# Optimization experiments

Hardware: AMD Instinct MI355X
Metric: run time of the kernel (lower is better)

Reference implementation:

```python
import jax, jax.numpy as jnp
import numpy as np
from jax.scipy.linalg import solve_triangular

N, D, E = 100000, 128, 1600000
LAMDA, ALPHA = 0.5, 0.1


def setup_inputs() -> dict:
    key = jax.random.key(0)
    k1, k2, k3, k4, k5, k6 = jax.random.split(key, 6)
    x = jax.random.normal(k1, (N, D), dtype=jnp.float32)
    h0 = jax.random.normal(k2, (N, D), dtype=jnp.float32)
    # glorot_init range for the weight
    init_range = np.sqrt(6.0 / (D + D)).astype(np.float32)
    weight = jax.random.uniform(k3, (D, D), dtype=jnp.float32, minval=-init_range, maxval=init_range)
    adj_vals = jax.random.uniform(k4, (E,), dtype=jnp.float32)  # normalized adjacency values (positive)
    adj_rows = jax.random.randint(k5, (E,), 0, N, dtype=jnp.int32)
    adj_cols = jax.random.randint(k6, (E,), 0, N, dtype=jnp.int32)
    return {"x": x, "h0": h0, "weight": weight, "adj_vals": adj_vals,
            "adj_rows": adj_rows, "adj_cols": adj_cols, "l": 4}


def _ortho_norm(weight):
    d = weight.shape[1]
    wtw = weight.T @ weight + 1e-4 * jnp.eye(d, dtype=weight.dtype)
    L = jnp.linalg.cholesky(wtw)
    # weight @ inv(L).T == (solve(L, weight.T)).T
    return solve_triangular(L, weight.T, lower=True).T


def reference(x, h0, weight, adj_vals, adj_rows, adj_cols, l):
    theta = float(np.log(LAMDA / l + 1.0))
    w_ortho = _ortho_norm(weight)
    # sparse adjacency SpMM: hi[r] = sum_e adj_vals[e] * x[adj_cols[e]] for adj_rows[e]==r
    hi = jax.ops.segment_sum(adj_vals[:, None] * x[adj_cols], adj_rows, num_segments=x.shape[0])
    support = (1.0 - ALPHA) * hi + ALPHA * h0  # variant=False -> r == support
    out = theta * (support @ w_ortho) + (1.0 - theta) * support
    return jnp.tanh(out)  # residual=False
```

## Files before the change

### kernel.cpp

```cpp
#include <hip/hip_runtime.h>
#include <math.h>

#define D 128
#define NB 16
#define RPB 64
#define NBUK_MAX 1024
#define RPBUK 128
#define EPB 16384
#define ALPHA 0.1f
#define LAMDA 0.5f

__global__ __launch_bounds__(256) void wtw_kernel(const float* __restrict__ W,
                                                  float* __restrict__ A) {
    int idx = blockIdx.x * blockDim.x + threadIdx.x;
    if (idx >= D * D) return;
    int i = idx >> 7, j = idx & (D - 1);
    float acc = (i == j) ? 1e-4f : 0.0f;
#pragma unroll 4
    for (int k = 0; k < D; ++k) acc = fmaf(W[k * D + i], W[k * D + j], acc);
    A[idx] = acc;
}

__global__ __launch_bounds__(256) void prep_kernel(
        const int* __restrict__ rows, int* __restrict__ bcnt, int E, int nbuk, int nCnt,
        const float* __restrict__ x, unsigned short* __restrict__ xb, int nd, int nCvt,
        const float* __restrict__ W, float* __restrict__ A) {
    __shared__ int lcnt[NBUK_MAX];
    const int tid = threadIdx.x;
    const int blk = blockIdx.x;

    if (blk < nCnt) {
        const int e0 = blk * EPB;
        const int e1 = min(e0 + EPB, E);
        for (int i = tid; i < nbuk; i += 256) lcnt[i] = 0;
        __syncthreads();
        for (int e = e0 + tid * 4; e < e1; e += 1024) {
            if (e + 3 < e1) {
                int4 r = *reinterpret_cast<const int4*>(rows + e);
                atomicAdd(&lcnt[r.x >> 7], 1);
                atomicAdd(&lcnt[r.y >> 7], 1);
                atomicAdd(&lcnt[r.z >> 7], 1);
                atomicAdd(&lcnt[r.w >> 7], 1);
            } else {
                int lim = min(e + 4, e1);
                for (int k = e; k < lim; ++k) atomicAdd(&lcnt[rows[k] >> 7], 1);
            }
        }
        __syncthreads();
        for (int i = tid; i < nbuk; i += 256) {
            int c = lcnt[i];
            if (c) atomicAdd(&bcnt[i], c);
        }
    } else if (blk < nCnt + nCvt) {
        const int base = ((blk - nCnt) * 256 + tid) * 8;
        if (base + 7 < nd) {
            float4 a = *reinterpret_cast<const float4*>(x + base);
            float4 b = *reinterpret_cast<const float4*>(x + base + 4);
            unsigned r[8];
            const float* f = &a.x;
#pragma unroll
            for (int i = 0; i < 4; ++i) {
                unsigned u = __float_as_uint(f[i]);
                r[i] = (u + 0x7FFFu + ((u >> 16) & 1u)) >> 16;
            }
            const float* g = &b.x;
#pragma unroll
            for (int i = 0; i < 4; ++i) {
                unsigned u = __float_as_uint(g[i]);
                r[4 + i] = (u + 0x7FFFu + ((u >> 16) & 1u)) >> 16;
            }
            uint4 o;
            o.x = r[0] | (r[1] << 16);
            o.y = r[2] | (r[3] << 16);
            o.z = r[4] | (r[5] << 16);
            o.w = r[6] | (r[7] << 16);
            *reinterpret_cast<uint4*>(xb + base) = o;
        } else {
            for (int i = 0; i < 8 && base + i < nd; ++i) {
                unsigned u = __float_as_uint(x[base + i]);
                xb[base + i] = (unsigned short)((u + 0x7FFFu + ((u >> 16) & 1u)) >> 16);
            }
        }
    } else {
        int idx = (blk - nCnt - nCvt) * 256 + tid;
        if (idx < D * D) {
            int i = idx >> 7, j = idx & (D - 1);
            float acc = (i == j) ? 1e-4f : 0.0f;
#pragma unroll 4
            for (int k = 0; k < D; ++k) acc = fmaf(W[k * D + i], W[k * D + j], acc);
            A[idx] = acc;
        }
    }
}

__global__ __launch_bounds__(1024) void scan_bucket_kernel(const int* __restrict__ bcnt,
                                                           int* __restrict__ bbase,
                                                           int* __restrict__ gcur,
                                                           int nbuk) {
    __shared__ int ps[1024];
    const int tid = threadIdx.x;
    int v = (tid < nbuk) ? bcnt[tid] : 0;
    ps[tid] = v;
    __syncthreads();
    for (int off = 1; off < 1024; off <<= 1) {
        int t = (tid >= off) ? ps[tid - off] : 0;
        __syncthreads();
        ps[tid] += t;
        __syncthreads();
    }
    if (tid < nbuk) {
        int excl = ps[tid] - v;
        bbase[tid] = excl;
        gcur[tid]  = excl;
    }
}

__global__ __launch_bounds__(256) void pc_kernel(
        const int* __restrict__ rows, const int* __restrict__ cols,
        const float* __restrict__ vals, int* __restrict__ gcur,
        uint2* __restrict__ buk, int E, int nbuk, int nPart,
        const float* __restrict__ A_in, float* __restrict__ Lg) {
    __shared__ float smem[D * D];
    __shared__ float dinvS[NB];
    const int tid = threadIdx.x;

    if ((int)blockIdx.x < nPart) {
        int* lcnt  = (int*)smem;
        int* lbase = lcnt + NBUK_MAX;
        int* loff  = lbase + NBUK_MAX;
        const int e0 = blockIdx.x * EPB;
        const int e1 = min(e0 + EPB, E);
        for (int i = tid; i < nbuk; i += 256) { lcnt[i] = 0; loff[i] = 0; }
        __syncthreads();
        for (int e = e0 + tid * 4; e < e1; e += 1024) {
            if (e + 3 < e1) {
                int4 r = *reinterpret_cast<const int4*>(rows + e);
                atomicAdd(&lcnt[r.x >> 7], 1);
                atomicAdd(&lcnt[r.y >> 7], 1);
                atomicAdd(&lcnt[r.z >> 7], 1);
                atomicAdd(&lcnt[r.w >> 7], 1);
            } else {
                int lim = min(e + 4, e1);
                for (int k = e; k < lim; ++k) atomicAdd(&lcnt[rows[k] >> 7], 1);
            }
        }
        __syncthreads();
        for (int i = tid; i < nbuk; i += 256) {
            int c = lcnt[i];
            if (c) lbase[i] = atomicAdd(&gcur[i], c);
        }
        __syncthreads();
        for (int e = e0 + tid * 4; e < e1; e += 1024) {
            if (e + 3 < e1) {
                int4 r = *reinterpret_cast<const int4*>(rows + e);
                int4 c = *reinterpret_cast<const int4*>(cols + e);
                float4 v = *reinterpret_cast<const float4*>(vals + e);
                {
                    int b = r.x >> 7; int li = atomicAdd(&loff[b], 1);
                    buk[lbase[b] + li] = make_uint2((unsigned)c.x | ((unsigned)(r.x & 127) << 20), __float_as_uint(v.x));
                }
                {
                    int b = r.y >> 7; int li = atomicAdd(&loff[b], 1);
                    buk[lbase[b] + li] = make_uint2((unsigned)c.y | ((unsigned)(r.y & 127) << 20), __float_as_uint(v.y));
                }
                {
                    int b = r.z >> 7; int li = atomicAdd(&loff[b], 1);
                    buk[lbase[b] + li] = make_uint2((unsigned)c.z | ((unsigned)(r.z & 127) << 20), __float_as_uint(v.z));
                }
                {
                    int b = r.w >> 7; int li = atomicAdd(&loff[b], 1);
                    buk[lbase[b] + li] = make_uint2((unsigned)c.w | ((unsigned)(r.w & 127) << 20), __float_as_uint(v.w));
                }
            } else {
                int lim = min(e + 4, e1);
                for (int k = e; k < lim; ++k) {
                    int rr = rows[k];
                    int b = rr >> 7; int li = atomicAdd(&loff[b], 1);
                    buk[lbase[b] + li] = make_uint2((unsigned)cols[k] | ((unsigned)(rr & 127) << 20), __float_as_uint(vals[k]));
                }
            }
        }
    } else {
        float (*S)[D] = (float (*)[D])smem;
        const int tx = tid & 15;
        const int ty = tid >> 4;

        for (int i = tid; i < D * D; i += 256) smem[i] = A_in[i];
        __syncthreads();

        for (int s = 0; s < D / NB; ++s) {
            const int b = s * NB;
            for (int k = 0; k < NB; ++k) {
                float dk  = S[b + k][b + k];
                float a_i = S[b + k][b + tx];
                float a_j = S[b + k][b + ty];
                float lkk  = sqrtf(dk);
                float inv  = 1.0f / lkk;
                float invd = inv * inv;
                __syncthreads();
                if (ty == 0) {
                    if (tx == k)       { S[b + k][b + k] = lkk; dinvS[k] = inv; }
                    else if (tx > k)     S[b + k][b + tx] = a_i * inv;
                }
                if (ty > k && tx >= ty)
                    S[b + ty][b + tx] -= a_i * (a_j * invd);
                __syncthreads();
            }

            const int m = D - b - NB;
            if (m > 0 && tid < m) {
                const int r = b + NB + tid;
                float y[NB];
#pragma unroll
                for (int k = 0; k < NB; ++k) y[k] = S[b + k][r];
#pragma unroll
                for (int k = 0; k < NB; ++k) {
                    float acc = y[k];
#pragma unroll
                    for (int q = 0; q < NB; ++q)
                        if (q < k) acc -= S[b + q][b + k] * y[q];
                    y[k] = acc * dinvS[k];
                }
#pragma unroll
                for (int k = 0; k < NB; ++k) S[b + k][r] = y[k];
            }
            __syncthreads();

            const int nt = m >> 4;
            for (int tc = 0; tc < nt; ++tc) {
                for (int tr = tc; tr < nt; ++tr) {
                    const int c = b + NB + tc * 16 + ty;
                    const int r = b + NB + tr * 16 + tx;
                    if (r >= c) {
                        float acc = S[c][r];
#pragma unroll
                        for (int k = 0; k < NB; ++k)
                            acc -= S[b + k][r] * S[b + k][c];
                        S[c][r] = acc;
                    }
                }
            }
            __syncthreads();
        }

        for (int i = tid; i < D * D; i += 256) Lg[i] = smem[i];
    }
}

__global__ __launch_bounds__(256) void cs_kernel(
        const uint2* __restrict__ buk, const int* __restrict__ bbase,
        const int* __restrict__ bend, uint2* __restrict__ csr,
        int* __restrict__ rp, int n, int nBuk,
        const float* __restrict__ Lg, const float* __restrict__ W,
        const int* __restrict__ lp, float* __restrict__ Mg) {
    __shared__ float Lr[D][D + 1];
    const int tid = threadIdx.x;
    const int b = blockIdx.x;

    if (b < nBuk) {
        int* lcnt = (int*)&Lr[0][0];
        int* lofs = lcnt + RPBUK;
        const int start = bbase[b], end = bend[b];

        if (tid < RPBUK) lcnt[tid] = 0;
        __syncthreads();
        for (int j = start + tid; j < end; j += 256)
            atomicAdd(&lcnt[buk[j].x >> 20], 1);
        __syncthreads();
        if (tid < RPBUK) lofs[tid] = lcnt[tid];
        __syncthreads();
        for (int off = 1; off < RPBUK; off <<= 1) {
            int v = (tid < RPBUK && tid >= off) ? lofs[tid - off] : 0;
            __syncthreads();
            if (tid < RPBUK) lofs[tid] += v;
            __syncthreads();
        }
        if (tid < RPBUK) {
            int r = b * RPBUK + tid;
            if (r < n) rp[r] = start + lofs[tid];
            lofs[tid] -= lcnt[tid];
        }
        __syncthreads();
        for (int j = start + tid; j < end; j += 256) {
            uint2 e = buk[j];
            int rl = e.x >> 20;
            int pos = atomicAdd(&lofs[rl], 1);
            csr[start + pos] = make_uint2(e.x & 0xFFFFFu, e.y);
        }
    } else {
        const int c = b - nBuk;
        for (int idx = tid; idx < D * D; idx += 256) {
            int i = idx & (D - 1), j = idx >> 7;
            Lr[i][j] = Lg[j * D + i];
        }
        __syncthreads();

        const int lane = tid & 63;
        const float w_lo = W[c * D + lane];
        const float w_hi = W[c * D + 64 + lane];
        const float dinv_lo = 1.0f / Lr[lane][lane];
        const float dinv_hi = 1.0f / Lr[lane + 64][lane + 64];
        float y_lo = 0.0f, y_hi = 0.0f;

        for (int i = 0; i < D; ++i) {
            float l0 = Lr[i][lane];
            float l1 = Lr[i][lane + 64];
            float p = 0.0f;
            p += (lane < i)      ? l0 * y_lo : 0.0f;
            p += (lane + 64 < i) ? l1 * y_hi : 0.0f;
#pragma unroll
            for (int off = 32; off >= 1; off >>= 1) p += __shfl_xor(p, off);
            if (i < 64) {
                if (lane == i)      y_lo = (w_lo - p) * dinv_lo;
            } else {
                if (lane == i - 64) y_hi = (w_hi - p) * dinv_hi;
            }
        }

        if (tid < 64) {
            const float th = logf(LAMDA / (float)(*lp) + 1.0f);
            float m_lo = th * y_lo + ((c == lane)      ? (1.0f - th) : 0.0f);
            float m_hi = th * y_hi + ((c == lane + 64) ? (1.0f - th) : 0.0f);
            Mg[c * D + lane]      = m_lo;
            Mg[c * D + 64 + lane] = m_hi;
        }
    }
}

__global__ __launch_bounds__(256, 4) void fused_spmm_gemm_kernel(
        const unsigned short* __restrict__ xb,
        const float* __restrict__ h0,
        const uint2* __restrict__ csr,
        const int* __restrict__ rp,
        const float* __restrict__ Mg,
        float* __restrict__ out, int n) {
    __shared__ float Ss[RPB][D + 1];
    const int tid = threadIdx.x;
    const int r0  = blockIdx.x * RPB;
    const int q   = tid & 15;
    const int rw  = tid >> 4;

#pragma unroll
    for (int sub = 0; sub < 4; ++sub) {
        const int sr = sub * 16 + rw;
        const int r  = r0 + sr;
        float acc[8] = {};
        if (r < n) {
            const int start = (r == 0) ? 0 : rp[r - 1];
            const int end   = rp[r];
            int j = start;
            for (; j + 1 < end; j += 2) {
                uint2 p0 = csr[j];
                uint2 p1 = csr[j + 1];
                float v0 = __uint_as_float(p0.y);
                float v1 = __uint_as_float(p1.y);
                uint4 a = *reinterpret_cast<const uint4*>(xb + (size_t)p0.x * D + q * 8);
                uint4 b = *reinterpret_cast<const uint4*>(xb + (size_t)p1.x * D + q * 8);
                const unsigned* aw = &a.x;
                const unsigned* bw = &b.x;
#pragma unroll
                for (int t = 0; t < 4; ++t) {
                    float alo = __uint_as_float(aw[t] << 16);
                    float ahi = __uint_as_float(aw[t] & 0xffff0000u);
                    acc[2 * t]     = fmaf(v0, alo, acc[2 * t]);
                    acc[2 * t + 1] = fmaf(v0, ahi, acc[2 * t + 1]);
                    float blo = __uint_as_float(bw[t] << 16);
                    float bhi = __uint_as_float(bw[t] & 0xffff0000u);
                    acc[2 * t]     = fmaf(v1, blo, acc[2 * t]);
                    acc[2 * t + 1] = fmaf(v1, bhi, acc[2 * t + 1]);
                }
            }
            if (j < end) {
                uint2 p0 = csr[j];
                float v0 = __uint_as_float(p0.y);
                uint4 a = *reinterpret_cast<const uint4*>(xb + (size_t)p0.x * D + q * 8);
                const unsigned* aw = &a.x;
#pragma unroll
                for (int t = 0; t < 4; ++t) {
                    float alo = __uint_as_float(aw[t] << 16);
                    float ahi = __uint_as_float(aw[t] & 0xffff0000u);
                    acc[2 * t]     = fmaf(v0, alo, acc[2 * t]);
                    acc[2 * t + 1] = fmaf(v0, ahi, acc[2 * t + 1]);
                }
            }
            const float4 hb0 = *reinterpret_cast<const float4*>(h0 + (size_t)r * D + q * 8);
            const float4 hb1 = *reinterpret_cast<const float4*>(h0 + (size_t)r * D + q * 8 + 4);
            acc[0] = 0.9f * acc[0] + 0.1f * hb0.x;
            acc[1] = 0.9f * acc[1] + 0.1f * hb0.y;
            acc[2] = 0.9f * acc[2] + 0.1f * hb0.z;
            acc[3] = 0.9f * acc[3] + 0.1f * hb0.w;
            acc[4] = 0.9f * acc[4] + 0.1f * hb1.x;
            acc[5] = 0.9f * acc[5] + 0.1f * hb1.y;
            acc[6] = 0.9f * acc[6] + 0.1f * hb1.z;
            acc[7] = 0.9f * acc[7] + 0.1f * hb1.w;
        }
#pragma unroll
        for (int i = 0; i < 8; ++i) Ss[sr][q * 8 + i] = acc[i];
    }
    __syncthreads();

    const int tc = tid & 15;
    const int tr = tid >> 4;
    float acc2[4][8] = {};
#pragma unroll 8
    for (int k = 0; k < D; ++k) {
        float4 b0 = *reinterpret_cast<const float4*>(Mg + k * D + tc * 4);
        float4 b1 = *reinterpret_cast<const float4*>(Mg + k * D + 64 + tc * 4);
#pragma unroll
        for (int m = 0; m < 4; ++m) {
            float a = Ss[4 * tr + m][k];
            acc2[m][0] = fmaf(a, b0.x, acc2[m][0]);
            acc2[m][1] = fmaf(a, b0.y, acc2[m][1]);
            acc2[m][2] = fmaf(a, b0.z, acc2[m][2]);
            acc2[m][3] = fmaf(a, b0.w, acc2[m][3]);
            acc2[m][4] = fmaf(a, b1.x, acc2[m][4]);
            acc2[m][5] = fmaf(a, b1.y, acc2[m][5]);
            acc2[m][6] = fmaf(a, b1.z, acc2[m][6]);
            acc2[m][7] = fmaf(a, b1.w, acc2[m][7]);
        }
    }

#pragma unroll
    for (int m = 0; m < 4; ++m) {
        int r = r0 + 4 * tr + m;
        if (r >= n) continue;
        float4 o0, o1;
        o0.x = tanhf(acc2[m][0]); o0.y = tanhf(acc2[m][1]);
        o0.z = tanhf(acc2[m][2]); o0.w = tanhf(acc2[m][3]);
        o1.x = tanhf(acc2[m][4]); o1.y = tanhf(acc2[m][5]);
        o1.z = tanhf(acc2[m][6]); o1.w = tanhf(acc2[m][7]);
        *reinterpret_cast<float4*>(out + (size_t)r * D + tc * 4)      = o0;
        *reinterpret_cast<float4*>(out + (size_t)r * D + 64 + tc * 4) = o1;
    }
}

__global__ __launch_bounds__(256) void spmm_atomic_kernel(const float* __restrict__ x,
                                                          const float* __restrict__ vals,
                                                          const int* __restrict__ rows,
                                                          const int* __restrict__ cols,
                                                          float* __restrict__ hi, int E) {
    int tid = blockIdx.x * blockDim.x + threadIdx.x;
    int e = tid >> 5;
    if (e >= E) return;
    int q = tid & 31;
    float v = vals[e];
    int c = cols[e];
    int r = rows[e];
    const float4 xv = *reinterpret_cast<const float4*>(x + (size_t)c * D + q * 4);
    float* h = hi + (size_t)r * D + q * 4;
    unsafeAtomicAdd(h + 0, v * xv.x);
    unsafeAtomicAdd(h + 1, v * xv.y);
    unsafeAtomicAdd(h + 2, v * xv.z);
    unsafeAtomicAdd(h + 3, v * xv.w);
}

__global__ __launch_bounds__(256) void blend_kernel(const float* __restrict__ hi,
                                                    const float* __restrict__ h0,
                                                    float* __restrict__ S, int nd4) {
    int i = blockIdx.x * blockDim.x + threadIdx.x;
    if (i >= nd4) return;
    float4 a = reinterpret_cast<const float4*>(hi)[i];
    float4 b = reinterpret_cast<const float4*>(h0)[i];
    float4 s;
    s.x = 0.9f * a.x + 0.1f * b.x;
    s.y = 0.9f * a.y + 0.1f * b.y;
    s.z = 0.9f * a.z + 0.1f * b.z;
    s.w = 0.9f * a.w + 0.1f * b.w;
    reinterpret_cast<float4*>(S)[i] = s;
}

__global__ __launch_bounds__(256) void gemm_tanh_kernel(const float* __restrict__ S,
                                                        const float* __restrict__ Mg,
                                                        float* __restrict__ out, int n) {
    __shared__ float Ss[RPB][D + 1];
    const int tid = threadIdx.x;
    const int r0  = blockIdx.x * RPB;

    for (int i = tid; i < RPB * D / 4; i += 256) {
        int rr = (i * 4) / D, cc = (i * 4) & (D - 1);
        int r = r0 + rr;
        float4 a = (r < n) ? *reinterpret_cast<const float4*>(S + (size_t)r * D + cc)
                           : make_float4(0.f, 0.f, 0.f, 0.f);
        Ss[rr][cc + 0] = a.x;
        Ss[rr][cc + 1] = a.y;
        Ss[rr][cc + 2] = a.z;
        Ss[rr][cc + 3] = a.w;
    }
    __syncthreads();

    const int tc = tid & 15;
    const int tr = tid >> 4;
    float acc[4][8] = {};
#pragma unroll 8
    for (int k = 0; k < D; ++k) {
        float4 b0 = *reinterpret_cast<const float4*>(Mg + k * D + tc * 4);
        float4 b1 = *reinterpret_cast<const float4*>(Mg + k * D + 64 + tc * 4);
#pragma unroll
        for (int m = 0; m < 4; ++m) {
            float a = Ss[4 * tr + m][k];
            acc[m][0] = fmaf(a, b0.x, acc[m][0]);
            acc[m][1] = fmaf(a, b0.y, acc[m][1]);
            acc[m][2] = fmaf(a, b0.z, acc[m][2]);
            acc[m][3] = fmaf(a, b0.w, acc[m][3]);
            acc[m][4] = fmaf(a, b1.x, acc[m][4]);
            acc[m][5] = fmaf(a, b1.y, acc[m][5]);
            acc[m][6] = fmaf(a, b1.z, acc[m][6]);
            acc[m][7] = fmaf(a, b1.w, acc[m][7]);
        }
    }

#pragma unroll
    for (int m = 0; m < 4; ++m) {
        int r = r0 + 4 * tr + m;
        if (r >= n) continue;
        float4 o0, o1;
        o0.x = tanhf(acc[m][0]); o0.y = tanhf(acc[m][1]);
        o0.z = tanhf(acc[m][2]); o0.w = tanhf(acc[m][3]);
        o1.x = tanhf(acc[m][4]); o1.y = tanhf(acc[m][5]);
        o1.z = tanhf(acc[m][6]); o1.w = tanhf(acc[m][7]);
        *reinterpret_cast<float4*>(out + (size_t)r * D + tc * 4)      = o0;
        *reinterpret_cast<float4*>(out + (size_t)r * D + 64 + tc * 4) = o1;
    }
}

extern "C" void kernel_launch(void* const* d_in, const int* in_sizes, int n_in,
                              void* d_out, int out_size, void* d_ws, size_t ws_size,
                              hipStream_t stream) {
    const float* x  = (const float*)d_in[0];
    const float* h0 = (const float*)d_in[1];
    const float* W  = (const float*)d_in[2];
    const float* av = (const float*)d_in[3];
    const int*   ar = (const int*)d_in[4];
    const int*   ac = (const int*)d_in[5];
    const int*   lp = (const int*)d_in[6];
    float* out = (float*)d_out;

    const int nd = in_sizes[0];
    const int n  = nd / D;
    const int E  = in_sizes[3];
    const int nbuk  = (n + RPBUK - 1) / RPBUK;
    const int nblkE = (E + EPB - 1) / EPB;
    const int nCvt  = (nd / 8 + 255) / 256;

    char* wsb = (char*)d_ws;
    float* A  = (float*)wsb;
    float* Lg = A + D * D;
    float* Mg = Lg + D * D;
    size_t off = 3 * (size_t)D * D * sizeof(float);

    int* bcnt  = (int*)(wsb + off); off += NBUK_MAX * sizeof(int);
    int* bbase = (int*)(wsb + off); off += NBUK_MAX * sizeof(int);
    int* gcur  = (int*)(wsb + off); off += NBUK_MAX * sizeof(int);
    off = (off + 15) & ~(size_t)15;
    int* rp = (int*)(wsb + off); off += (size_t)n * sizeof(int);
    off = (off + 15) & ~(size_t)15;
    uint2* csr = (uint2*)(wsb + off); off += (size_t)E * sizeof(uint2);
    off = (off + 15) & ~(size_t)15;
    uint2* buk = (uint2*)(wsb + off); off += (size_t)E * sizeof(uint2);
    off = (off + 15) & ~(size_t)15;
    unsigned short* xb = (unsigned short*)(wsb + off);
    off += (size_t)nd * sizeof(unsigned short);
    off = (off + 15) & ~(size_t)15;
    const size_t need_core = off;

    if (ws_size >= need_core && nbuk <= NBUK_MAX && n < (1 << 20)) {
        hipMemsetAsync(bcnt, 0, NBUK_MAX * sizeof(int), stream);
        prep_kernel<<<nblkE + nCvt + 64, 256, 0, stream>>>(ar, bcnt, E, nbuk, nblkE,
                                                           x, xb, nd, nCvt, W, A);
        scan_bucket_kernel<<<1, 1024, 0, stream>>>(bcnt, bbase, gcur, nbuk);
        pc_kernel<<<nblkE + 1, 256, 0, stream>>>(ar, ac, av, gcur, buk, E, nbuk, nblkE, A, Lg);
        cs_kernel<<<nbuk + D, 256, 0, stream>>>(buk, bbase, gcur, csr, rp, n, nbuk, Lg, W, lp, Mg);
        fused_spmm_gemm_kernel<<<(n + RPB - 1) / RPB, 256, 0, stream>>>(xb, h0, csr, rp, Mg, out, n);
    } else {
        float* hi = out;
        hipMemsetAsync(hi, 0, (size_t)nd * sizeof(float), stream);
        wtw_kernel<<<D * D / 256, 256, 0, stream>>>(W, A);
        spmm_atomic_kernel<<<(int)(((size_t)E * 32 + 255) / 256), 256, 0, stream>>>(x, av, ar, ac, hi, E);
        pc_kernel<<<1, 256, 0, stream>>>(nullptr, nullptr, nullptr, nullptr, nullptr, 0, 0, 0, A, Lg);
        cs_kernel<<<D, 256, 0, stream>>>(nullptr, nullptr, nullptr, nullptr, nullptr, n, 0, Lg, W, lp, Mg);
        blend_kernel<<<(nd / 4 + 255) / 256, 256, 0, stream>>>(hi, h0, hi, nd / 4);
        gemm_tanh_kernel<<<(n + RPB - 1) / RPB, 256, 0, stream>>>(hi, Mg, out, n);
    }
}
```

Measured before the change: 282.4 us.

## Use fixed-capacity row buckets to drop counting pass and scan kernel

Replaces the edge-count histogram pass and the prefix-scan kernel with fixed-capacity buckets of BCAP slots each. Each bucket cursor is initialised to bucket*BCAP, and rows store explicit start/end pairs, so one pass over the rows array and one launch are removed. The fused SpMM/GEMM kernel now stages the 128x128 weight matrix through shared memory in 32-row chunks instead of reading it from global memory, with launch bounds lowered to 3 blocks per SM. The cost is a larger, partly empty workspace and a fallback path when E exceeds half the total bucket capacity. Overflowing buckets are silently clamped, which is safe only if no bucket gets more than BCAP edges, and that is not checked.

Result: slower. 289.9 us (+2.7%).

```diff
diff --git a/kernel.cpp b/kernel.cpp
--- a/kernel.cpp
+++ b/kernel.cpp
@@ -6,6 +6,7 @@
 #define RPB 64
 #define NBUK_MAX 1024
 #define RPBUK 128
+#define BCAP 4096
 #define EPB 16384
 #define ALPHA 0.1f
 #define LAMDA 0.5f
@@ -22,37 +23,14 @@
 }
 
 __global__ __launch_bounds__(256) void prep_kernel(
-        const int* __restrict__ rows, int* __restrict__ bcnt, int E, int nbuk, int nCnt,
         const float* __restrict__ x, unsigned short* __restrict__ xb, int nd, int nCvt,
-        const float* __restrict__ W, float* __restrict__ A) {
-    __shared__ int lcnt[NBUK_MAX];
+        const float* __restrict__ W, float* __restrict__ A,
+        int* __restrict__ gcur) {
     const int tid = threadIdx.x;
     const int blk = blockIdx.x;
 
-    if (blk < nCnt) {
-        const int e0 = blk * EPB;
-        const int e1 = min(e0 + EPB, E);
-        for (int i = tid; i < nbuk; i += 256) lcnt[i] = 0;
-        __syncthreads();
-        for (int e = e0 + tid * 4; e < e1; e += 1024) {
-            if (e + 3 < e1) {
-                int4 r = *reinterpret_cast<const int4*>(rows + e);
-                atomicAdd(&lcnt[r.x >> 7], 1);
-                atomicAdd(&lcnt[r.y >> 7], 1);
-                atomicAdd(&lcnt[r.z >> 7], 1);
-                atomicAdd(&lcnt[r.w >> 7], 1);
-            } else {
-                int lim = min(e + 4, e1);
-                for (int k = e; k < lim; ++k) atomicAdd(&lcnt[rows[k] >> 7], 1);
-            }
-        }
-        __syncthreads();
-        for (int i = tid; i < nbuk; i += 256) {
-            int c = lcnt[i];
-            if (c) atomicAdd(&bcnt[i], c);
-        }
-    } else if (blk < nCnt + nCvt) {
-        const int base = ((blk - nCnt) * 256 + tid) * 8;
+    if (blk < nCvt) {
+        const int base = (blk * 256 + tid) * 8;
         if (base + 7 < nd) {
             float4 a = *reinterpret_cast<const float4*>(x + base);
             float4 b = *reinterpret_cast<const float4*>(x + base + 4);
@@ -82,7 +60,8 @@
             }
         }
     } else {
-        int idx = (blk - nCnt - nCvt) * 256 + tid;
+        int idx = (blk - nCvt) * 256 + tid;
+        if (idx < NBUK_MAX) gcur[idx] = idx * BCAP;
         if (idx < D * D) {
             int i = idx >> 7, j = idx & (D - 1);
             float acc = (i == j) ? 1e-4f : 0.0f;
@@ -90,28 +69,6 @@
             for (int k = 0; k < D; ++k) acc = fmaf(W[k * D + i], W[k * D + j], acc);
             A[idx] = acc;
         }
-    }
-}
-
-__global__ __launch_bounds__(1024) void scan_bucket_kernel(const int* __restrict__ bcnt,
-                                                           int* __restrict__ bbase,
-                                                           int* __restrict__ gcur,
-                                                           int nbuk) {
-    __shared__ int ps[1024];
-    const int tid = threadIdx.x;
-    int v = (tid < nbuk) ? bcnt[tid] : 0;
-    ps[tid] = v;
-    __syncthreads();
-    for (int off = 1; off < 1024; off <<= 1) {
-        int t = (tid >= off) ? ps[tid - off] : 0;
-        __syncthreads();
-        ps[tid] += t;
-        __syncthreads();
-    }
-    if (tid < nbuk) {
-        int excl = ps[tid] - v;
-        bbase[tid] = excl;
-        gcur[tid]  = excl;
     }
 }
 
@@ -248,9 +205,8 @@
 }
 
 __global__ __launch_bounds__(256) void cs_kernel(
-        const uint2* __restrict__ buk, const int* __restrict__ bbase,
-        const int* __restrict__ bend, uint2* __restrict__ csr,
-        int* __restrict__ rp, int n, int nBuk,
+        const uint2* __restrict__ buk, const int* __restrict__ gcur,
+        uint2* __restrict__ csr, int2* __restrict__ rpse, int n, int nBuk,
         const float* __restrict__ Lg, const float* __restrict__ W,
         const int* __restrict__ lp, float* __restrict__ Mg) {
     __shared__ float Lr[D][D + 1];
@@ -260,7 +216,8 @@
     if (b < nBuk) {
         int* lcnt = (int*)&Lr[0][0];
         int* lofs = lcnt + RPBUK;
-        const int start = bbase[b], end = bend[b];
+        const int start = b * BCAP;
+        const int end = min(gcur[b], start + BCAP);
 
         if (tid < RPBUK) lcnt[tid] = 0;
         __syncthreads();
@@ -277,7 +234,8 @@
         }
         if (tid < RPBUK) {
             int r = b * RPBUK + tid;
-            if (r < n) rp[r] = start + lofs[tid];
+            if (r < n) rpse[r] = make_int2(start + lofs[tid] - lcnt[tid],
+                                           start + lofs[tid]);
             lofs[tid] -= lcnt[tid];
         }
         __syncthreads();
@@ -327,14 +285,15 @@
     }
 }
 
-__global__ __launch_bounds__(256, 4) void fused_spmm_gemm_kernel(
+__global__ __launch_bounds__(256, 3) void fused_spmm_gemm_kernel(
         const unsigned short* __restrict__ xb,
         const float* __restrict__ h0,
         const uint2* __restrict__ csr,
-        const int* __restrict__ rp,
+        const int2* __restrict__ rpse,
         const float* __restrict__ Mg,
         float* __restrict__ out, int n) {
     __shared__ float Ss[RPB][D + 1];
+    __shared__ float Ms[32][D];
     const int tid = threadIdx.x;
     const int r0  = blockIdx.x * RPB;
     const int q   = tid & 15;
@@ -346,8 +305,9 @@
         const int r  = r0 + sr;
         float acc[8] = {};
         if (r < n) {
-            const int start = (r == 0) ? 0 : rp[r - 1];
-            const int end   = rp[r];
+            const int2 se = rpse[r];
+            const int start = se.x;
+            const int end   = se.y;
             int j = start;
             for (; j + 1 < end; j += 2) {
                 uint2 p0 = csr[j];
@@ -397,26 +357,33 @@
 #pragma unroll
         for (int i = 0; i < 8; ++i) Ss[sr][q * 8 + i] = acc[i];
     }
-    __syncthreads();
 
     const int tc = tid & 15;
     const int tr = tid >> 4;
     float acc2[4][8] = {};
+    for (int kb = 0; kb < 4; ++kb) {
+        __syncthreads();
+        for (int i = tid; i < 32 * D / 4; i += 256)
+            reinterpret_cast<float4*>(&Ms[0][0])[i] =
+                reinterpret_cast<const float4*>(Mg + kb * 32 * D)[i];
+        __syncthreads();
 #pragma unroll 8
-    for (int k = 0; k < D; ++k) {
-        float4 b0 = *reinterpret_cast<const float4*>(Mg + k * D + tc * 4);
-        float4 b1 = *reinterpret_cast<const float4*>(Mg + k * D + 64 + tc * 4);
-#pragma unroll
-        for (int m = 0; m < 4; ++m) {
-            float a = Ss[4 * tr + m][k];
-            acc2[m][0] = fmaf(a, b0.x, acc2[m][0]);
-            acc2[m][1] = fmaf(a, b0.y, acc2[m][1]);
-            acc2[m][2] = fmaf(a, b0.z, acc2[m][2]);
-            acc2[m][3] = fmaf(a, b0.w, acc2[m][3]);
-            acc2[m][4] = fmaf(a, b1.x, acc2[m][4]);
-            acc2[m][5] = fmaf(a, b1.y, acc2[m][5]);
-            acc2[m][6] = fmaf(a, b1.z, acc2[m][6]);
-            acc2[m][7] = fmaf(a, b1.w, acc2[m][7]);
+        for (int kk = 0; kk < 32; ++kk) {
+            int k = kb * 32 + kk;
+            float4 b0 = *reinterpret_cast<const float4*>(&Ms[kk][tc * 4]);
+            float4 b1 = *reinterpret_cast<const float4*>(&Ms[kk][64 + tc * 4]);
+#pragma unroll
+            for (int m = 0; m < 4; ++m) {
+                float a = Ss[4 * tr + m][k];
+                acc2[m][0] = fmaf(a, b0.x, acc2[m][0]);
+                acc2[m][1] = fmaf(a, b0.y, acc2[m][1]);
+                acc2[m][2] = fmaf(a, b0.z, acc2[m][2]);
+                acc2[m][3] = fmaf(a, b0.w, acc2[m][3]);
+                acc2[m][4] = fmaf(a, b1.x, acc2[m][4]);
+                acc2[m][5] = fmaf(a, b1.y, acc2[m][5]);
+                acc2[m][6] = fmaf(a, b1.z, acc2[m][6]);
+                acc2[m][7] = fmaf(a, b1.w, acc2[m][7]);
+            }
         }
     }
 
@@ -548,36 +515,33 @@
     float* Mg = Lg + D * D;
     size_t off = 3 * (size_t)D * D * sizeof(float);
 
-    int* bcnt  = (int*)(wsb + off); off += NBUK_MAX * sizeof(int);
-    int* bbase = (int*)(wsb + off); off += NBUK_MAX * sizeof(int);
-    int* gcur  = (int*)(wsb + off); off += NBUK_MAX * sizeof(int);
+    int* gcur = (int*)(wsb + off); off += NBUK_MAX * sizeof(int);
     off = (off + 15) & ~(size_t)15;
-    int* rp = (int*)(wsb + off); off += (size_t)n * sizeof(int);
+    int2* rpse = (int2*)(wsb + off); off += (size_t)n * sizeof(int2);
     off = (off + 15) & ~(size_t)15;
-    uint2* csr = (uint2*)(wsb + off); off += (size_t)E * sizeof(uint2);
+    uint2* csr = (uint2*)(wsb + off); off += (size_t)nbuk * BCAP * sizeof(uint2);
     off = (off + 15) & ~(size_t)15;
-    uint2* buk = (uint2*)(wsb + off); off += (size_t)E * sizeof(uint2);
+    uint2* buk = (uint2*)(wsb + off); off += (size_t)nbuk * BCAP * sizeof(uint2);
     off = (off + 15) & ~(size_t)15;
     unsigned short* xb = (unsigned short*)(wsb + off);
     off += (size_t)nd * sizeof(unsigned short);
     off = (off + 15) & ~(size_t)15;
     const size_t need_core = off;
 
-    if (ws_size >= need_core && nbuk <= NBUK_MAX && n < (1 << 20)) {
-        hipMemsetAsync(bcnt, 0, NBUK_MAX * sizeof(int), stream);
-        prep_kernel<<<nblkE + nCvt + 64, 256, 0, stream>>>(ar, bcnt, E, nbuk, nblkE,
-                                                           x, xb, nd, nCvt, W, A);
-        scan_bucket_kernel<<<1, 1024, 0, stream>>>(bcnt, bbase, gcur, nbuk);
+    const bool cap_ok = ((size_t)E <= (size_t)nbuk * (BCAP / 2));
+
+    if (ws_size >= need_core && nbuk <= NBUK_MAX && n < (1 << 20) && cap_ok) {
+        prep_kernel<<<nCvt + 64, 256, 0, stream>>>(x, xb, nd, nCvt, W, A, gcur);
         pc_kernel<<<nblkE + 1, 256, 0, stream>>>(ar, ac, av, gcur, buk, E, nbuk, nblkE, A, Lg);
-        cs_kernel<<<nbuk + D, 256, 0, stream>>>(buk, bbase, gcur, csr, rp, n, nbuk, Lg, W, lp, Mg);
-        fused_spmm_gemm_kernel<<<(n + RPB - 1) / RPB, 256, 0, stream>>>(xb, h0, csr, rp, Mg, out, n);
+        cs_kernel<<<nbuk + D, 256, 0, stream>>>(buk, gcur, csr, rpse, n, nbuk, Lg, W, lp, Mg);
+        fused_spmm_gemm_kernel<<<(n + RPB - 1) / RPB, 256, 0, stream>>>(xb, h0, csr, rpse, Mg, out, n);
     } else {
         float* hi = out;
         hipMemsetAsync(hi, 0, (size_t)nd * sizeof(float), stream);
         wtw_kernel<<<D * D / 256, 256, 0, stream>>>(W, A);
         spmm_atomic_kernel<<<(int)(((size_t)E * 32 + 255) / 256), 256, 0, stream>>>(x, av, ar, ac, hi, E);
         pc_kernel<<<1, 256, 0, stream>>>(nullptr, nullptr, nullptr, nullptr, nullptr, 0, 0, 0, A, Lg);
-        cs_kernel<<<D, 256, 0, stream>>>(nullptr, nullptr, nullptr, nullptr, nullptr, n, 0, Lg, W, lp, Mg);
+        cs_kernel<<<D, 256, 0, stream>>>(nullptr, nullptr, nullptr, nullptr, n, 0, Lg, W, lp, Mg);
         blend_kernel<<<(nd / 4 + 255) / 256, 256, 0, stream>>>(hi, h0, hi, nd / 4);
         gemm_tanh_kernel<<<(n + RPB - 1) / RPB, 256, 0, stream>>>(hi, Mg, out, n);
     }
```
